# Optimization experiments

Measured on AMD Instinct MI355X. Metric: run time of the kernel, lower is better.

## Reference

```python
import jax, jax.numpy as jnp
import numpy as np

B = 2097152  # batch
H = 9        # hidden width
N_MID = 19   # fc2..fc20


def setup_inputs() -> dict:
    key = jax.random.key(0)
    ks = jax.random.split(key, 8)
    x = jax.random.normal(ks[0], (B, 2), dtype=jnp.float32)
    # PyTorch Linear init: U(-1/sqrt(fan_in), 1/sqrt(fan_in))
    def lin(k, out_f, in_f):
        kw, kb = jax.random.split(k)
        bound = 1.0 / np.sqrt(in_f)
        W = jax.random.uniform(kw, (out_f, in_f), jnp.float32, -bound, bound)
        b = jax.random.uniform(kb, (out_f,), jnp.float32, -bound, bound)
        return W, b
    W1, b1 = lin(ks[1], H, 2)
    # stacked middle layers fc2..fc20: [19, 9, 9] / [19, 9]
    kmids = jax.random.split(ks[2], N_MID)
    Wmid = jnp.stack([lin(k, H, H)[0] for k in kmids])
    bmid = jnp.stack([lin(jax.random.fold_in(k, 1), H, H)[1] for k in kmids])
    W21, b21 = lin(ks[3], 2, H)
    return {"x": x, "W1": W1, "b1": b1, "Wmid": Wmid, "bmid": bmid,
            "W21": W21, "b21": b21}


def reference(x, W1, b1, Wmid, bmid, W21, b21):
    h = jax.nn.elu(x @ W1.T + b1)  # [B, 9]
    def layer(h, wb):
        W, b = wb
        return jax.nn.elu(h @ W.T + b), None
    h, _ = jax.lax.scan(layer, h, (Wmid, bmid))
    logits = h @ W21.T + b21  # [B, 2]
    return jax.nn.log_softmax(logits, axis=1)
```

## Files before the change

kernel.cpp:

```cpp
#include <hip/hip_runtime.h>


typedef _Float16 half8 __attribute__((ext_vector_type(8)));
typedef _Float16 h2 __attribute__((ext_vector_type(2)));
typedef float float4v __attribute__((ext_vector_type(4)));
typedef unsigned int uint4v __attribute__((ext_vector_type(4)));

extern "C" __device__ _Float16 __ocml_exp2_f16(_Float16);

constexpr int H   = 9;
constexpr int NL  = 21;
constexpr int TPW = 8;
constexpr int BLK = 256;

__global__ void build_frags(const float* __restrict__ W1, const float* __restrict__ b1,
                            const float* __restrict__ Wmid, const float* __restrict__ bmid,
                            const float* __restrict__ W21, const float* __restrict__ b21,
                            _Float16* __restrict__ ws) {
    const float L   = 1.4426950408889634f;
    const float LN2 = 0.6931471805599453f;
    int l    = blockIdx.x;
    int lane = threadIdx.x;
    int row  = lane & 15;
    int g    = lane >> 4;
    bool orow = ((row & 3) != 3) && (row < 12);
    int  o    = row - (row >> 2);
    for (int j = 0; j < 8; ++j) {
        int k = g * 8 + j;
        float v = 0.0f;
        if (l == 0) {
            if (orow && k < 2)        v = L * W1[o * 2 + k];
            else if (orow && k == 24) v = L * b1[o];
        } else if (l <= 19) {
            const float* W = Wmid + (l - 1) * 81;
            const float* b = bmid + (l - 1) * 9;
            if (orow) {
                if (j < 3 && g < 3) {
                    int r_in = g * 4 + j;
                    int i = r_in - (r_in >> 2);
                    v = W[o * 9 + i];
                } else if (j >= 4 && j < 7 && g < 3) {
                    int r_in = g * 4 + (j - 4);
                    int i = r_in - (r_in >> 2);
                    v = L * W[o * 9 + i];
                } else if (k == 24) {
                    float s = 0.0f;
                    for (int i = 0; i < H; ++i) s += W[o * 9 + i];
                    v = L * (b[o] - s);
                }
            }
        } else {
            if (row < 2) {
                if (j < 3 && g < 3) {
                    int r_in = g * 4 + j;
                    int i = r_in - (r_in >> 2);
                    v = LN2 * W21[row * 9 + i];
                } else if (j >= 4 && j < 7 && g < 3) {
                    int r_in = g * 4 + (j - 4);
                    int i = r_in - (r_in >> 2);
                    v = W21[row * 9 + i];
                } else if (k == 24) {
                    float s = 0.0f;
                    for (int i = 0; i < H; ++i) s += W21[row * 9 + i];
                    v = b21[row] - s;
                }
            }
        }
        ws[l * 512 + lane * 8 + j] = (_Float16)v;
    }
}

__device__ __forceinline__ half8 act_to_b(float4v d, unsigned bias_or) {
    const h2 Z = {(_Float16)0.f, (_Float16)0.f};
    h2 p01 = __builtin_bit_cast(h2, __builtin_amdgcn_cvt_pkrtz(d[0], d[1]));
    h2 p2x = __builtin_bit_cast(h2, __builtin_amdgcn_cvt_pkrtz(d[2], d[3]));
    h2 r01 = __builtin_elementwise_max(p01, Z);
    h2 r2x = __builtin_elementwise_max(p2x, Z);
    h2 t01 = __builtin_elementwise_min(p01, Z);
    h2 t2x = __builtin_elementwise_min(p2x, Z);
    h2 e01;
    e01[0] = __ocml_exp2_f16(t01[0]);
    e01[1] = __ocml_exp2_f16(t01[1]);
    h2 e2x = t2x;
    e2x[0] = __ocml_exp2_f16(t2x[0]);
    uint4v u;
    u[0] = __builtin_bit_cast(unsigned, r01) | bias_or;
    u[1] = __builtin_bit_cast(unsigned, r2x);
    u[2] = __builtin_bit_cast(unsigned, e01);
    u[3] = __builtin_bit_cast(unsigned, e2x);
    return __builtin_bit_cast(half8, u);
}

__device__ __forceinline__ half8 x_to_b(float2 xv, unsigned g0_sel, unsigned bias_or) {
    unsigned ux = __builtin_bit_cast(unsigned, __builtin_amdgcn_cvt_pkrtz(xv.x, xv.y));
    uint4v u;
    u[0] = (ux & g0_sel) | bias_or;
    u[1] = 0u; u[2] = 0u; u[3] = 0u;
    return __builtin_bit_cast(half8, u);
}

__device__ __forceinline__ void write_out(float4v d, float* __restrict__ out,
                                          long long row, int lane) {
    if (lane < 16) {
        float l0 = d[0], l1 = d[1];
        float m  = fmaxf(l0, l1);
        float e0 = __expf(l0 - m);
        float e1 = __expf(l1 - m);
        float lse = m + __logf(e0 + e1);
        ((float2*)out)[row] = make_float2(l0 - lse, l1 - lse);
    }
}

__global__ __launch_bounds__(BLK) void mlp_mfma(const float* __restrict__ x,
                                                const _Float16* __restrict__ ws,
                                                float* __restrict__ out) {
    const int lane = threadIdx.x & 63;
    const int wave = (blockIdx.x * BLK + threadIdx.x) >> 6;
    const int grp  = lane >> 4;
    const int col  = lane & 15;

    half8 A[NL];
    const half8* wsv = (const half8*)ws;
    #pragma unroll
    for (int l = 0; l < NL; ++l) A[l] = wsv[l * 64 + lane];

    const unsigned bias_or = (grp == 3) ? 0x00003C00u : 0u;
    const unsigned g0_sel  = (grp == 0) ? 0xFFFFFFFFu : 0u;

    #pragma unroll 1
    for (int t = 0; t < TPW; t += 2) {
        const long long rowa = ((long long)wave * TPW + t) * 16 + col;
        const long long rowb = rowa + 16;

        float2 xa = ((const float2*)x)[rowa];
        float2 xb = ((const float2*)x)[rowb];
        half8 ba = x_to_b(xa, g0_sel, bias_or);
        half8 bb = x_to_b(xb, g0_sel, bias_or);

        float4v da, db;
        #pragma unroll
        for (int l = 0; l < NL; ++l) {
            da = __builtin_amdgcn_mfma_f32_16x16x32_f16(A[l], ba, (float4v){0.f,0.f,0.f,0.f}, 0, 0, 0);
            db = __builtin_amdgcn_mfma_f32_16x16x32_f16(A[l], bb, (float4v){0.f,0.f,0.f,0.f}, 0, 0, 0);
            if (l < NL - 1) {
                ba = act_to_b(da, bias_or);
                bb = act_to_b(db, bias_or);
            }
        }
        write_out(da, out, rowa, lane);
        write_out(db, out, rowb, lane);
    }
}

extern "C" void kernel_launch(void* const* d_in, const int* in_sizes, int n_in,
                              void* d_out, int out_size, void* d_ws, size_t ws_size,
                              hipStream_t stream) {
    const float* x    = (const float*)d_in[0];
    const float* W1   = (const float*)d_in[1];
    const float* b1   = (const float*)d_in[2];
    const float* Wmid = (const float*)d_in[3];
    const float* bmid = (const float*)d_in[4];
    const float* W21  = (const float*)d_in[5];
    const float* b21  = (const float*)d_in[6];
    float* out = (float*)d_out;
    _Float16* ws = (_Float16*)d_ws;

    build_frags<<<NL, 64, 0, stream>>>(W1, b1, Wmid, bmid, W21, b21, ws);

    const int nrows = in_sizes[0] / 2;
    const int tiles = nrows / 16;
    const int waves = tiles / TPW;
    const int blocks = waves * 64 / BLK;
    mlp_mfma<<<blocks, BLK, 0, stream>>>(x, ws, out);
}
```

Measured before the change: 179.1 us.

## Interleave four MFMA tiles per wave and spread softmax epilogue across all lanes

Each wave now processes four 16-row tiles at once instead of two, so four independent MFMA chains per layer can hide MFMA and activation latency. The log-softmax epilogue gathers each tile's two logits into a different 16-lane group with ds_bpermute, so all 64 lanes do the math and write one coalesced 64-row store instead of four partial-lane stores. The softmax uses a single exp2/log form on the absolute logit difference. The cost is more live registers for the four accumulators and B fragments, which may lower occupancy.

After: 176.1 us. Within noise of the previous version (-1.7%).

```diff
diff --git a/kernel.cpp b/kernel.cpp
--- a/kernel.cpp
+++ b/kernel.cpp
@@ -99,16 +99,9 @@
     return __builtin_bit_cast(half8, u);
 }
 
-__device__ __forceinline__ void write_out(float4v d, float* __restrict__ out,
-                                          long long row, int lane) {
-    if (lane < 16) {
-        float l0 = d[0], l1 = d[1];
-        float m  = fmaxf(l0, l1);
-        float e0 = __expf(l0 - m);
-        float e1 = __expf(l1 - m);
-        float lse = m + __logf(e0 + e1);
-        ((float2*)out)[row] = make_float2(l0 - lse, l1 - lse);
-    }
+__device__ __forceinline__ float bperm(int byte_idx, float v) {
+    return __builtin_bit_cast(float,
+        __builtin_amdgcn_ds_bpermute(byte_idx, __builtin_bit_cast(int, v)));
 }
 
 __global__ __launch_bounds__(BLK) void mlp_mfma(const float* __restrict__ x,
@@ -126,29 +119,48 @@
 
     const unsigned bias_or = (grp == 3) ? 0x00003C00u : 0u;
     const unsigned g0_sel  = (grp == 0) ? 0xFFFFFFFFu : 0u;
+    const float4v ZV = {0.f, 0.f, 0.f, 0.f};
+    const float NLOG2E = -1.4426950408889634f;
+    const float LN2f   = 0.6931471805599453f;
 
     #pragma unroll 1
-    for (int t = 0; t < TPW; t += 2) {
-        const long long rowa = ((long long)wave * TPW + t) * 16 + col;
-        const long long rowb = rowa + 16;
+    for (int t = 0; t < TPW; t += 4) {
+        const int tile0 = wave * TPW + t;
 
-        float2 xa = ((const float2*)x)[rowa];
-        float2 xb = ((const float2*)x)[rowb];
-        half8 ba = x_to_b(xa, g0_sel, bias_or);
-        half8 bb = x_to_b(xb, g0_sel, bias_or);
+        half8 bf[4];
+        #pragma unroll
+        for (int k = 0; k < 4; ++k) {
+            float2 xv = ((const float2*)x)[((tile0 + k) << 4) + col];
+            bf[k] = x_to_b(xv, g0_sel, bias_or);
+        }
 
-        float4v da, db;
+        float4v dd[4];
         #pragma unroll
         for (int l = 0; l < NL; ++l) {
-            da = __builtin_amdgcn_mfma_f32_16x16x32_f16(A[l], ba, (float4v){0.f,0.f,0.f,0.f}, 0, 0, 0);
-            db = __builtin_amdgcn_mfma_f32_16x16x32_f16(A[l], bb, (float4v){0.f,0.f,0.f,0.f}, 0, 0, 0);
+            #pragma unroll
+            for (int k = 0; k < 4; ++k)
+                dd[k] = __builtin_amdgcn_mfma_f32_16x16x32_f16(A[l], bf[k], ZV, 0, 0, 0);
             if (l < NL - 1) {
-                ba = act_to_b(da, bias_or);
-                bb = act_to_b(db, bias_or);
+                #pragma unroll
+                for (int k = 0; k < 4; ++k)
+                    bf[k] = act_to_b(dd[k], bias_or);
             }
         }
-        write_out(da, out, rowa, lane);
-        write_out(db, out, rowb, lane);
+
+        const int bidx = col << 2;
+        float a0 = bperm(bidx, dd[0][0]), a1 = bperm(bidx, dd[0][1]);
+        float b0 = bperm(bidx, dd[1][0]), b1 = bperm(bidx, dd[1][1]);
+        float c0 = bperm(bidx, dd[2][0]), c1 = bperm(bidx, dd[2][1]);
+        float d0 = bperm(bidx, dd[3][0]), d1 = bperm(bidx, dd[3][1]);
+        float l0 = (grp == 0) ? a0 : (grp == 1) ? b0 : (grp == 2) ? c0 : d0;
+        float l1 = (grp == 0) ? a1 : (grp == 1) ? b1 : (grp == 2) ? c1 : d1;
+
+        float mx  = fmaxf(l0, l1);
+        float ad  = fabsf(l0 - l1);
+        float e   = __builtin_amdgcn_exp2f(NLOG2E * ad);
+        float lg  = __builtin_amdgcn_logf(1.0f + e);
+        float lse = fmaf(LN2f, lg, mx);
+        ((float2*)out)[(tile0 << 4) + lane] = make_float2(l0 - lse, l1 - lse);
     }
 }
 
```
